# Optimization experiments

Hardware: AMD Instinct MI355X
Metric: run time of the kernel (lower is better)

The kernel has to match this reference:

```python
import jax, jax.numpy as jnp
import numpy as np
from jax import lax

S, B, XD, AD, ZD, K, H = 128, 32, 1024, 8, 4, 3, 50
CN = 32 * 3 * 3
DN = ('NCHW', 'OIHW', 'NCHW')


def setup_inputs():
    key = jax.random.key(0)
    ks = jax.random.split(key, 20)
    g = lambda k, sh, s=0.1: jax.random.normal(k, sh, dtype=jnp.float32) * s
    z = lambda n: jnp.zeros((n,), jnp.float32)
    return {
        'x': jax.random.uniform(ks[0], (S, B, XD), dtype=jnp.float32),
        'eps': jax.random.normal(ks[1], (S, B, AD), dtype=jnp.float32),
        'Wc0': g(ks[2], (32, 1, 3, 3)), 'bc0': z(32),
        'Wc1': g(ks[3], (32, 32, 3, 3)), 'bc1': z(32),
        'Wc2': g(ks[4], (32, 32, 3, 3)), 'bc2': z(32),
        'Wm': g(ks[5], (AD, CN)), 'bm': z(AD),
        'Wlv': g(ks[6], (AD, CN)), 'blv': z(AD),
        'Wd': g(ks[7], (CN, AD)), 'bd': z(CN),
        'Wt0': g(ks[8], (32, 32, 3, 3)), 'bt0': z(32),
        'Wt1': g(ks[9], (32, 32, 3, 3)), 'bt1': z(32),
        'Wt2': g(ks[10], (32, 32, 3, 3)), 'bt2': z(32),
        'Wg': g(ks[11], (32, 1, 1, 1)), 'bg': z(1),
        'A': jnp.tile(jnp.eye(ZD, dtype=jnp.float32)[None], (K, 1, 1)),
        'Bm': g(ks[12], (K, ZD, AD), 0.05),
        'Cm': g(ks[13], (K, AD, ZD), 0.05),
        'a_init': jnp.zeros((1, AD), jnp.float32),
        'W_ih': g(ks[14], (4 * H, AD)), 'W_hh': g(ks[15], (4 * H, H)),
        'b_ih': z(4 * H), 'b_hh': z(4 * H),
        'Wa': g(ks[16], (K, H)), 'ba': z(K),
    }


def _conv(h, W, b):
    y = lax.conv_general_dilated(h, W, (2, 2), 'VALID', dimension_numbers=DN)
    return y + b[None, :, None, None]


def _convT(h, W, b, op):
    # PyTorch ConvTranspose2d(k=3, stride=2, padding=0, output_padding=op)
    Wf = jnp.transpose(jnp.flip(W, (2, 3)), (1, 0, 2, 3))
    pad = (2, 2 + op)
    y = lax.conv_general_dilated(h, Wf, (1, 1), [pad, pad], lhs_dilation=(2, 2), dimension_numbers=DN)
    return y + b[None, :, None, None]


def _forward(x, eps, Wc0, bc0, Wc1, bc1, Wc2, bc2, Wm, bm, Wlv, blv, Wd, bd,
             Wt0, bt0, Wt1, bt1, Wt2, bt2, Wg, bg, A, Bm, Cm, a_init,
             W_ih, W_hh, b_ih, b_hh, Wa, ba):
    relu, sig = jax.nn.relu, jax.nn.sigmoid
    # ---- encode: x -> a ----
    xf = x.reshape(S * B, 1, 32, 32)
    h = relu(_conv(xf, Wc0, bc0))          # (SB,32,15,15)
    h = relu(_conv(h, Wc1, bc1))           # (SB,32,7,7)
    h = relu(_conv(h, Wc2, bc2))           # (SB,32,3,3)
    feat = h.reshape(S, B, CN)
    a_mean = feat @ Wm.T + bm
    a_logvar = sig(feat @ Wlv.T + blv)
    a = a_mean + eps * jnp.exp(0.5 * a_logvar)
    # ---- decode: a -> log_y ----
    d = (a.reshape(S * B, AD) @ Wd.T + bd).reshape(S * B, 32, 3, 3)
    d = relu(_convT(d, Wt0, bt0, 0))       # (SB,32,7,7)
    d = relu(_convT(d, Wt1, bt1, 0))       # (SB,32,15,15)
    d = relu(_convT(d, Wt2, bt2, 1))       # (SB,32,32,32)
    log_y = sig(jnp.einsum('nchw,c->nhw', d, Wg[:, 0, 0, 0]) + bg[0]).reshape(S, B, XD)
    # ---- alpha from a_{t-1} via LSTM ----
    a_tm1 = jnp.concatenate([jnp.broadcast_to(a_init[:, None, :], (1, B, AD)), a[:-1]], 0)
    def lstm_step(carry, xt):
        h_, c_ = carry
        gates = xt @ W_ih.T + b_ih + h_ @ W_hh.T + b_hh
        i, f, gg, o = jnp.split(gates, 4, axis=-1)
        c_ = sig(f) * c_ + sig(i) * jnp.tanh(gg)
        h_ = sig(o) * jnp.tanh(c_)
        return (h_, c_), h_
    _, hs = lax.scan(lstm_step, (jnp.zeros((B, H), jnp.float32), jnp.zeros((B, H), jnp.float32)), a_tm1)
    alpha = jax.nn.softmax(hs @ Wa.T + ba, axis=-1)     # (S,B,K)
    A_mix = jnp.einsum('sbk,kij->sbij', alpha, A)
    B_mix = jnp.einsum('sbk,kij->sbij', alpha, Bm)
    C_mix = jnp.einsum('sbk,kij->sbij', alpha, Cm)
    u = a_tm1
    # ---- Kalman filter ----
    Qm = 0.08 * jnp.eye(ZD, dtype=jnp.float32)
    Rm = 0.03 * jnp.eye(AD, dtype=jnp.float32)
    Iz = jnp.eye(ZD, dtype=jnp.float32)
    mu0 = jnp.zeros((B, ZD), jnp.float32)
    Sigma0 = 20.0 * jnp.tile(Iz[None], (B, 1, 1))
    def filt(carry, xs):
        mu, Sig = carry
        A_t, B_t, C_t, a_t, u_t, first = xs
        mu_p = jnp.einsum('bij,bj->bi', A_t, mu) + jnp.einsum('bij,bj->bi', B_t, u_t)
        Sig_p = A_t @ Sig @ jnp.swapaxes(A_t, 1, 2) + Qm
        mu_p = jnp.where(first, mu0, mu_p)
        Sig_p = jnp.where(first, Sigma0, Sig_p)
        res = a_t - jnp.einsum('bij,bj->bi', C_t, mu_p)
        S_ = C_t @ Sig_p @ jnp.swapaxes(C_t, 1, 2) + Rm
        Kt = Sig_p @ jnp.swapaxes(C_t, 1, 2) @ jnp.linalg.inv(S_)
        mu_f = mu_p + jnp.einsum('bij,bj->bi', Kt, res)
        IKC = Iz - Kt @ C_t
        Sig_f = IKC @ Sig_p @ jnp.swapaxes(IKC, 1, 2) + Kt @ Rm @ jnp.swapaxes(Kt, 1, 2)
        return (mu_f, Sig_f), (mu_p, mu_f, Sig_p, Sig_f)
    first = jnp.arange(S) == 0
    _, (mu_pred, mu_filt, Sig_pred, Sig_filt) = lax.scan(filt, (mu0, Sigma0), (A_mix, B_mix, C_mix, a, u, first))
    # ---- RTS smoother ----
    def smooth(carry, xs):
        mu_s, Sig_s = carry
        Sf, A_n, Sp_n, muf, muf_n = xs
        J = Sf @ jnp.swapaxes(A_n, 1, 2) @ jnp.linalg.inv(Sp_n)
        mu_new = muf + jnp.einsum('bij,bj->bi', J, mu_s - muf_n)
        Sig_new = Sf + J @ (Sig_s - Sp_n) @ jnp.swapaxes(J, 1, 2)
        return (mu_new, Sig_new), (mu_new, Sig_new)
    _, (mu_sm, Sig_sm) = lax.scan(smooth, (mu_filt[-1], Sig_filt[-1]),
                                  (Sig_filt[:-1], A_mix[1:], Sig_pred[1:], mu_filt[:-1], mu_filt[1:]),
                                  reverse=True)
    mu_smooth = jnp.concatenate([mu_sm, mu_filt[-1:]], 0)
    Sigma_smooth = jnp.concatenate([Sig_sm, Sig_filt[-1:]], 0)
    return log_y, a, a_mean, a_logvar, mu_smooth, Sigma_smooth


def reference(x, eps, Wc0, bc0, Wc1, bc1, Wc2, bc2, Wm, bm, Wlv, blv, Wd, bd,
              Wt0, bt0, Wt1, bt1, Wt2, bt2, Wg, bg, A, Bm, Cm, a_init,
              W_ih, W_hh, b_ih, b_hh, Wa, ba):
    return _forward(x, eps, Wc0, bc0, Wc1, bc1, Wc2, bc2, Wm, bm, Wlv, blv, Wd, bd,
                    Wt0, bt0, Wt1, bt1, Wt2, bt2, Wg, bg, A, Bm, Cm, a_init,
                    W_ih, W_hh, b_ih, b_hh, Wa, ba)
```

## Files before the change

kernel.cpp:

```cpp
#include <hip/hip_runtime.h>
#include <math.h>

#define DI __device__ __forceinline__

DI float sigm(float x){ return 1.0f/(1.0f+__expf(-x)); }
DI float tanhx(float x){ float ax=fabsf(x); float e=__expf(2.0f*ax); float t=1.0f-2.0f/(e+1.0f); return copysignf(t,x); }
DI unsigned short f2bf(float x){ unsigned u=__float_as_uint(x); return (unsigned short)((u+0x7fffu+((u>>16)&1u))>>16); }

typedef __attribute__((ext_vector_type(8))) short bf16x8;
typedef __attribute__((ext_vector_type(4))) float f32x4;
#define MFMA16(a,b,c) __builtin_amdgcn_mfma_f32_16x16x32_bf16(a,b,c,0,0,0)

static constexpr int RS  = 296;
static constexpr int RSZ = 9472;
static constexpr int AS  = 40;

static constexpr size_t OFF_A   = 4194304;
static constexpr size_t OFF_AM  = OFF_A   + 32768;
static constexpr size_t OFF_ALV = OFF_AM  + 32768;
static constexpr size_t OFF_MU  = OFF_ALV + 32768;
static constexpr size_t OFF_SG  = OFF_MU  + 16384;

DI float inv4_lane(float Mv, int r, int c){
  int a0=(c==0)?1:0, a1=(c<=1)?2:1, a2=(c<=2)?3:2;
  int b0=(r==0)?1:0, b1=(r<=1)?2:1, b2=(r<=2)?3:2;
  float m00=__shfl(Mv,(a0<<3)|b0,64), m01=__shfl(Mv,(a0<<3)|b1,64), m02=__shfl(Mv,(a0<<3)|b2,64);
  float m10=__shfl(Mv,(a1<<3)|b0,64), m11=__shfl(Mv,(a1<<3)|b1,64), m12=__shfl(Mv,(a1<<3)|b2,64);
  float m20=__shfl(Mv,(a2<<3)|b0,64), m21=__shfl(Mv,(a2<<3)|b1,64), m22=__shfl(Mv,(a2<<3)|b2,64);
  float det3 = m00*(m11*m22-m12*m21) - m01*(m10*m22-m12*m20) + m02*(m10*m21-m11*m20);
  float adj = (((r+c)&1)? -det3 : det3);
  float det=0.f;
  #pragma unroll
  for(int i=0;i<4;i++)
    det += __shfl(Mv,(i<<3),64)*__shfl(adj,i,64);
  return adj*(1.0f/det);
}

DI void inv4_serial(const float* m, float* o){
  float i0 = m[5]*m[10]*m[15]-m[5]*m[11]*m[14]-m[9]*m[6]*m[15]+m[9]*m[7]*m[14]+m[13]*m[6]*m[11]-m[13]*m[7]*m[10];
  float i4 = -m[4]*m[10]*m[15]+m[4]*m[11]*m[14]+m[8]*m[6]*m[15]-m[8]*m[7]*m[14]-m[12]*m[6]*m[11]+m[12]*m[7]*m[10];
  float i8 = m[4]*m[9]*m[15]-m[4]*m[11]*m[13]-m[8]*m[5]*m[15]+m[8]*m[7]*m[13]+m[12]*m[5]*m[11]-m[12]*m[7]*m[9];
  float i12= -m[4]*m[9]*m[14]+m[4]*m[10]*m[13]+m[8]*m[5]*m[14]-m[8]*m[6]*m[13]-m[12]*m[5]*m[10]+m[12]*m[6]*m[9];
  float i1 = -m[1]*m[10]*m[15]+m[1]*m[11]*m[14]+m[9]*m[2]*m[15]-m[9]*m[3]*m[14]-m[13]*m[2]*m[11]+m[13]*m[3]*m[10];
  float i5 = m[0]*m[10]*m[15]-m[0]*m[11]*m[14]-m[8]*m[2]*m[15]+m[8]*m[3]*m[14]+m[12]*m[2]*m[11]-m[12]*m[3]*m[10];
  float i9 = -m[0]*m[9]*m[15]+m[0]*m[11]*m[13]+m[8]*m[1]*m[15]-m[8]*m[3]*m[13]-m[12]*m[1]*m[11]+m[12]*m[3]*m[9];
  float i13= m[0]*m[9]*m[14]-m[0]*m[10]*m[13]-m[8]*m[1]*m[14]+m[8]*m[2]*m[13]+m[12]*m[1]*m[10]-m[12]*m[2]*m[9];
  float i2 = m[1]*m[6]*m[15]-m[1]*m[7]*m[14]-m[5]*m[2]*m[15]+m[5]*m[3]*m[14]+m[13]*m[2]*m[7]-m[13]*m[3]*m[6];
  float i6 = -m[0]*m[6]*m[15]+m[0]*m[7]*m[14]+m[4]*m[2]*m[15]-m[4]*m[3]*m[14]-m[12]*m[2]*m[7]+m[12]*m[3]*m[6];
  float i10= m[0]*m[5]*m[15]-m[0]*m[7]*m[13]-m[4]*m[1]*m[15]+m[4]*m[3]*m[13]+m[12]*m[1]*m[7]-m[12]*m[3]*m[5];
  float i14= -m[0]*m[5]*m[14]+m[0]*m[6]*m[13]+m[4]*m[1]*m[14]-m[4]*m[2]*m[13]-m[12]*m[1]*m[6]+m[12]*m[2]*m[5];
  float i3 = -m[1]*m[6]*m[11]+m[1]*m[7]*m[10]+m[5]*m[2]*m[11]-m[5]*m[3]*m[10]-m[9]*m[2]*m[7]+m[9]*m[3]*m[6];
  float i7 = m[0]*m[6]*m[11]-m[0]*m[7]*m[10]-m[4]*m[2]*m[11]+m[4]*m[3]*m[10]+m[8]*m[2]*m[7]-m[8]*m[3]*m[6];
  float i11= -m[0]*m[5]*m[11]+m[0]*m[7]*m[9]+m[4]*m[1]*m[11]-m[4]*m[3]*m[9]-m[8]*m[1]*m[7]+m[8]*m[3]*m[5];
  float i15= m[0]*m[5]*m[10]-m[0]*m[6]*m[9]-m[4]*m[1]*m[10]+m[4]*m[2]*m[9]+m[8]*m[1]*m[6]-m[8]*m[2]*m[5];
  float rd=1.0f/(m[0]*i0+m[1]*i4+m[2]*i8+m[3]*i12);
  o[0]=i0*rd; o[1]=i1*rd; o[2]=i2*rd; o[3]=i3*rd;
  o[4]=i4*rd; o[5]=i5*rd; o[6]=i6*rd; o[7]=i7*rd;
  o[8]=i8*rd; o[9]=i9*rd; o[10]=i10*rd; o[11]=i11*rd;
  o[12]=i12*rd; o[13]=i13*rd; o[14]=i14*rd; o[15]=i15*rd;
}

__global__ __launch_bounds__(256) void k_prep(
    const float* __restrict__ Wc1, const float* __restrict__ Wc2,
    const float* __restrict__ Wt0, const float* __restrict__ Wt1, const float* __restrict__ Wt2,
    unsigned short* __restrict__ ws16)
{
  int idx = blockIdx.x*256 + threadIdx.x;
  int mat = idx/RSZ, rem = idx%RSZ;
  int co = rem/RS, t = rem%RS;
  float v = 0.f;
  if (t < 288){
    int tap = t>>5, ci = t&31;
    if      (mat==0) v = Wc1[co*288+ci*9+tap];
    else if (mat==1) v = Wc2[co*288+ci*9+tap];
    else if (mat==2) v = Wt0[ci*288+co*9+tap];
    else if (mat==3) v = Wt1[ci*288+co*9+tap];
    else             v = Wt2[ci*288+co*9+tap];
  }
  ws16[idx] = f2bf(v);
}

struct EncSh {
  alignas(16) float img[1024];
  alignas(16) unsigned short h0T[9040];
  alignas(16) unsigned short h1T[2000];
  alignas(16) unsigned short BT1e[9472];
  alignas(16) unsigned short BT2e[9472];
  alignas(16) float feat[288];
};

__global__ __launch_bounds__(256) void k_enc(
    const float* __restrict__ x, const float* __restrict__ eps,
    const float* __restrict__ Wc0, const float* __restrict__ bc0,
    const float* __restrict__ bc1, const float* __restrict__ bc2,
    const float* __restrict__ Wm, const float* __restrict__ bm,
    const float* __restrict__ Wlv, const float* __restrict__ blv,
    const unsigned short* __restrict__ ws16,
    float* __restrict__ out)
{
  __shared__ EncSh E;
  const int n = blockIdx.x, tid = threadIdx.x;
  const int lane = tid & 63, wave = tid >> 6, g = lane >> 4, c15 = lane & 15;

  for (int i=tid;i<1024;i+=256) E.img[i]=x[(size_t)n*1024+i];
  {
    uint4* dst=(uint4*)E.BT1e;
    const uint4* src=(const uint4*)ws16;
    for (int i=tid;i<2368;i+=256) dst[i]=src[i];
  }
  if (tid<32){ E.h0T[225*AS+tid]=0; E.h1T[49*AS+tid]=0; }
  __syncthreads();

  for (int i=tid;i<7200;i+=256){
    int co=i&31, p=i>>5, oy=p/15, ox=p%15;
    float acc=bc0[co];
    const float* wp=Wc0+co*9;
    int base=2*oy*32+2*ox;
    #pragma unroll
    for(int ky=0;ky<3;ky++)
      #pragma unroll
      for(int kx=0;kx<3;kx++)
        acc += E.img[base+ky*32+kx]*wp[ky*3+kx];
    E.h0T[p*AS+co]=f2bf(fmaxf(acc,0.0f));
  }
  __syncthreads();

  {
    const int mt=wave;
    const int oy=mt*2+(c15>>3), ox=c15&7;
    f32x4 acc0={0.f,0.f,0.f,0.f}, acc1={0.f,0.f,0.f,0.f};
    #pragma unroll 1
    for (int ky=0;ky<3;ky++){
      #pragma unroll
      for (int kx=0;kx<3;kx++){
        int iy=2*oy+ky, ix=2*ox+kx;
        int pix=(iy<15&&ix<15)?(iy*15+ix):225;
        bf16x8 af=*(const bf16x8*)&E.h0T[pix*AS+g*8];
        int tap=ky*3+kx;
        bf16x8 b0=*(const bf16x8*)&E.BT1e[c15*RS+tap*32+g*8];
        bf16x8 b1=*(const bf16x8*)&E.BT1e[(c15+16)*RS+tap*32+g*8];
        acc0=MFMA16(af,b0,acc0);
        acc1=MFMA16(af,b1,acc1);
      }
    }
    float bA=bc1[c15], bB=bc1[c15+16];
    #pragma unroll
    for (int r=0;r<4;r++){
      int p16=g*4+r, oy2=mt*2+(p16>>3), ox2=p16&7;
      if (oy2<7 && ox2<7){
        E.h1T[(oy2*7+ox2)*AS+c15]   =f2bf(fmaxf(acc0[r]+bA,0.f));
        E.h1T[(oy2*7+ox2)*AS+c15+16]=f2bf(fmaxf(acc1[r]+bB,0.f));
      }
    }
  }
  __syncthreads();

  if (wave<2){
    const int nt=wave;
    const int valid=(c15<9);
    const int oy=c15/3, ox=c15-oy*3;
    f32x4 acc={0.f,0.f,0.f,0.f};
    #pragma unroll 1
    for (int ky=0;ky<3;ky++){
      #pragma unroll
      for (int kx=0;kx<3;kx++){
        int pix=valid?((2*oy+ky)*7+(2*ox+kx)):49;
        bf16x8 af=*(const bf16x8*)&E.h1T[pix*AS+g*8];
        int tap=ky*3+kx;
        bf16x8 bfr=*(const bf16x8*)&E.BT2e[(nt*16+c15)*RS+tap*32+g*8];
        acc=MFMA16(af,bfr,acc);
      }
    }
    float bb=bc2[nt*16+c15];
    #pragma unroll
    for (int r=0;r<4;r++){
      int p16=g*4+r;
      if (p16<9) E.feat[(nt*16+c15)*9+p16]=fmaxf(acc[r]+bb,0.f);
    }
  }
  __syncthreads();

  if (tid<64){
    const int j=tid>>3, kk=tid&7;
    float s1=0.f,s2=0.f;
    const float* wm=Wm+j*288;
    const float* wl=Wlv+j*288;
    #pragma unroll 6
    for(int m=kk*36;m<kk*36+36;m++){ float f=E.feat[m]; s1+=f*wm[m]; s2+=f*wl[m]; }
    #pragma unroll
    for(int d=4;d>0;d>>=1){ s1+=__shfl_down(s1,d,64); s2+=__shfl_down(s2,d,64); }
    if(kk==0){
      size_t o=(size_t)n*8+j;
      float am=s1+bm[j];
      float lv=sigm(s2+blv[j]);
      float av=am+eps[o]*__expf(0.5f*lv);
      out[OFF_AM+o]=am;
      out[OFF_ALV+o]=lv;
      out[OFF_A+o]=av;
    }
  }
}

struct DecSh {
  alignas(16) float aa[8];
  alignas(16) unsigned short d0T[400];
  alignas(16) unsigned short t0T[2000];
  alignas(16) unsigned short t1T[9040];
  alignas(16) unsigned short BT0[9472];
  alignas(16) unsigned short BT1[9472];
  alignas(16) unsigned short BT2[9472];
};
struct SeqSh {
  float a_loc[1024];
  float a0[8];
  float h[52];
  float gates[200];
  float wa[152];
  float w2[8][60];
  float logit[4];
  float alpha[384];
  float muf[512];
  float Sigf[2048];
  float Sigp[2048];
  float Jb[2048];
  float Amat[48];
};
union MainSh { DecSh d; SeqSh q; };

DI void kf_step(SeqSh& Q, int ks, int r, int c, bool aid,
                float At3[3], float Bt3[3], float Ct3[3],
                float& mu0, float& mu1, float& mu2, float& mu3, float& Sg)
{
  float al0=Q.alpha[ks*3+0], al1=Q.alpha[ks*3+1], al2=Q.alpha[ks*3+2];
  float At=al0*At3[0]+al1*At3[1]+al2*At3[2];
  float Bt=al0*Bt3[0]+al1*Bt3[1]+al2*Bt3[2];
  float Ct=al0*Ct3[0]+al1*Ct3[1]+al2*Ct3[2];
  float Mc=0.f;
  #pragma unroll
  for(int m=0;m<8;m++) Mc+=__shfl(Ct,(m<<3)|r,64)*__shfl(Ct,(m<<3)|c,64);
  float mp0,mp1,mp2,mp3;
  {
    float uc=(ks==0)?Q.a0[c]:Q.a_loc[(ks-1)*8+c];
    float vB=Bt*uc;
    vB+=__shfl_xor(vB,1,64); vB+=__shfl_xor(vB,2,64); vB+=__shfl_xor(vB,4,64);
    if (aid){
      mp0=mu0+__shfl(vB,0,64); mp1=mu1+__shfl(vB,8,64);
      mp2=mu2+__shfl(vB,16,64); mp3=mu3+__shfl(vB,24,64);
    } else {
      float mcc=(c==0)?mu0:((c==1)?mu1:((c==2)?mu2:((c==3)?mu3:0.f)));
      float vA=At*mcc;
      vA+=__shfl_xor(vA,1,64); vA+=__shfl_xor(vA,2,64);
      float comb=vA+vB;
      mp0=__shfl(comb,0,64); mp1=__shfl(comb,8,64);
      mp2=__shfl(comb,16,64); mp3=__shfl(comb,24,64);
    }
  }
  float Sp;
  if (aid){
    Sp=Sg+((r==c)?0.08f:0.f);
  } else {
    float T=0.f;
    #pragma unroll
    for(int k=0;k<4;k++) T+=__shfl(At,(r<<3)|k,64)*__shfl(Sg,(k<<3)|c,64);
    float sp=0.f;
    #pragma unroll
    for(int k=0;k<4;k++) sp+=__shfl(T,(r<<3)|k,64)*__shfl(At,(c<<3)|k,64);
    Sp=sp+((r==c)?0.08f:0.f);
  }
  if (ks==0){ mp0=0;mp1=0;mp2=0;mp3=0; Sp=(r==c)?20.f:0.f; }
  if (r<4&&c<4) Q.Sigp[ks*16+r*4+c]=Sp;
  float rr;
  {
    float mpc=(c==0)?mp0:((c==1)?mp1:((c==2)?mp2:((c==3)?mp3:0.f)));
    float v=Ct*mpc;
    v+=__shfl_xor(v,1,64); v+=__shfl_xor(v,2,64);
    rr=Q.a_loc[ks*8+r]-v;
  }
  float Spi=inv4_lane(Sp,r,c);
  float Mm=Spi+Mc*(1.0f/0.03f);
  float Sf=inv4_lane(Mm,r,c);
  if (r<4&&c<4) Q.Sigf[ks*16+r*4+c]=Sf;
  float Kq=0.f;
  #pragma unroll
  for(int k=0;k<4;k++) Kq+=__shfl(Sf,(r<<3)|k,64)*__shfl(Ct,(c<<3)|k,64);
  Kq*=(1.0f/0.03f);
  float resc=__shfl(rr,c<<3,64);
  float vv=Kq*resc;
  vv+=__shfl_xor(vv,1,64); vv+=__shfl_xor(vv,2,64); vv+=__shfl_xor(vv,4,64);
  float mufr=((r==0)?mp0:((r==1)?mp1:((r==2)?mp2:mp3)))+vv;
  float nm0=__shfl(mufr,0,64), nm1=__shfl(mufr,8,64), nm2=__shfl(mufr,16,64), nm3=__shfl(mufr,24,64);
  if (r<4&&c==0) Q.muf[ks*4+r]=mufr;
  mu0=nm0; mu1=nm1; mu2=nm2; mu3=nm3; Sg=Sf;
}

__global__ __launch_bounds__(512) void k_main(
    const float* __restrict__ Wd, const float* __restrict__ bd,
    const float* __restrict__ bt0, const float* __restrict__ bt1, const float* __restrict__ bt2,
    const float* __restrict__ Wg, const float* __restrict__ bgp,
    const float* __restrict__ Ag, const float* __restrict__ Bg, const float* __restrict__ Cg,
    const float* __restrict__ a_init,
    const float* __restrict__ W_ih, const float* __restrict__ W_hh,
    const float* __restrict__ b_ih, const float* __restrict__ b_hh,
    const float* __restrict__ Wa, const float* __restrict__ ba,
    const unsigned short* __restrict__ ws16,
    float* __restrict__ out)
{
  __shared__ MainSh sh;
  const int tid=threadIdx.x;
  const float* aglob = out + OFF_A;

  if (blockIdx.x < 32){
    if (tid>=256) return;
    SeqSh& Q = sh.q;
    const int b=blockIdx.x;
    for (int i=tid;i<1024;i+=256){ int s=i>>3, j=i&7; Q.a_loc[i]=aglob[((size_t)s*32+b)*8+j]; }
    if (tid<8)   Q.a0[tid]=a_init[tid];
    if (tid<150) Q.wa[tid]=Wa[tid];
    if (tid<52)  Q.h[tid]=0.f;
    if (tid>=208 && tid<256) Q.Amat[tid-208]=Ag[tid-208];
    for (int i=tid;i<464;i+=256){
      int rr2=i/58, k=i%58;
      Q.w2[rr2][k]=(k<8)? W_ih[(192+rr2)*8+k] : W_hh[(192+rr2)*50+(k-8)];
    }
    if (tid<8) Q.w2[tid][58]=b_ih[192+tid]+b_hh[192+tid];

    const int gr = tid-64;
    float wr[50], wi[8], bsum=0.f, creg=0.f;
    if (tid>=64){
      #pragma unroll
      for(int k=0;k<50;k++) wr[k]=W_hh[gr*50+k];
      #pragma unroll
      for(int j=0;j<8;j++) wi[j]=W_ih[gr*8+j];
      bsum=b_ih[gr]+b_hh[gr];
    }
    const int r=tid>>3, c=tid&7;
    float At3[3]={0,0,0}, Bt3[3]={0,0,0}, Ct3[3]={0,0,0};
    float mu0=0,mu1=0,mu2=0,mu3=0, Sg=0.f;
    bool aid=false;
    if (tid<64){
      if (r<4&&c<4){ At3[0]=Ag[r*4+c]; At3[1]=Ag[16+r*4+c]; At3[2]=Ag[32+r*4+c]; }
      if (r<4){ Bt3[0]=Bg[r*8+c]; Bt3[1]=Bg[32+r*8+c]; Bt3[2]=Bg[64+r*8+c]; }
      if (c<4){ Ct3[0]=Cg[r*4+c]; Ct3[1]=Cg[32+r*4+c]; Ct3[2]=Cg[64+r*4+c]; }
      int ok=1;
      if (r<4&&c<4){
        float d=(r==c)?1.f:0.f;
        ok=(At3[0]==d)&&(At3[1]==d)&&(At3[2]==d);
      }
      aid=(bool)__all(ok);
    }
    __syncthreads();

    for (int s=0;s<128;s++){
      if (tid>=64){
        float aA=bsum, aB=0.f;
        const float* ap=(s==0)?Q.a0:(Q.a_loc+(s-1)*8);
        #pragma unroll
        for(int j=0;j<8;j++) aA+=ap[j]*wi[j];
        #pragma unroll
        for(int k=0;k<50;k+=2){ aA+=Q.h[k]*wr[k]; aB+=Q.h[k+1]*wr[k+1]; }
        Q.gates[gr]=aA+aB;
        if (gr<8){
          const float* wp=Q.w2[gr];
          float s2=wp[58];
          #pragma unroll
          for(int j=0;j<8;j++) s2+=ap[j]*wp[j];
          #pragma unroll 10
          for(int k=0;k<50;k++) s2+=Q.h[k]*wp[8+k];
          Q.gates[192+gr]=s2;
        } else if (gr>=16 && gr<19 && s>0){
          int j=gr-16;
          float lv=ba[j];
          const float* wap=&Q.wa[j*50];
          #pragma unroll 5
          for(int k=0;k<50;k++) lv+=Q.h[k]*wap[k];
          Q.logit[j]=lv;
        }
      } else if (s>=2){
        kf_step(Q,s-2,r,c,aid,At3,Bt3,Ct3,mu0,mu1,mu2,mu3,Sg);
      }
      __syncthreads();
      if (tid>=64 && tid<114){
        int j=gr;
        float ig=sigm(Q.gates[j]);
        float fg=sigm(Q.gates[50+j]);
        float gg=tanhx(Q.gates[100+j]);
        float og=sigm(Q.gates[150+j]);
        creg=fg*creg+ig*gg;
        Q.h[j]=og*tanhx(creg);
      } else if (tid>=114 && tid<117 && s>0){
        int j=tid-114;
        float l0=Q.logit[0], l1=Q.logit[1], l2=Q.logit[2];
        float mx=fmaxf(l0,fmaxf(l1,l2));
        float e0=__expf(l0-mx), e1=__expf(l1-mx), e2=__expf(l2-mx);
        float lj=(j==0)?l0:((j==1)?l1:l2);
        Q.alpha[(s-1)*3+j]=__expf(lj-mx)/(e0+e1+e2);
      }
      __syncthreads();
    }
    if (tid<64){
      kf_step(Q,126,r,c,aid,At3,Bt3,Ct3,mu0,mu1,mu2,mu3,Sg);
    } else if (tid<67){
      int j=tid-64;
      float lv=ba[j];
      const float* wap=&Q.wa[j*50];
      #pragma unroll 5
      for(int k=0;k<50;k++) lv+=Q.h[k]*wap[k];
      Q.logit[j]=lv;
    }
    __syncthreads();
    if (tid>=64 && tid<67){
      int j=tid-64;
      float l0=Q.logit[0], l1=Q.logit[1], l2=Q.logit[2];
      float mx=fmaxf(l0,fmaxf(l1,l2));
      float e0=__expf(l0-mx), e1=__expf(l1-mx), e2=__expf(l2-mx);
      float lj=(j==0)?l0:((j==1)?l1:l2);
      Q.alpha[127*3+j]=__expf(lj-mx)/(e0+e1+e2);
    }
    __syncthreads();
    if (tid<64) kf_step(Q,127,r,c,aid,At3,Bt3,Ct3,mu0,mu1,mu2,mu3,Sg);
    __syncthreads();
    if (tid<127){
      const int n2=tid;
      float al0=Q.alpha[(n2+1)*3+0], al1=Q.alpha[(n2+1)*3+1], al2=Q.alpha[(n2+1)*3+2];
      float An[16], Sp[16], Spi[16], Sf[16], T[16];
      #pragma unroll
      for(int k=0;k<16;k++){
        An[k]=al0*Q.Amat[k]+al1*Q.Amat[16+k]+al2*Q.Amat[32+k];
        Sp[k]=Q.Sigp[(n2+1)*16+k];
        Sf[k]=Q.Sigf[n2*16+k];
      }
      inv4_serial(Sp,Spi);
      #pragma unroll
      for(int r2=0;r2<4;r2++)
        #pragma unroll
        for(int c2=0;c2<4;c2++){
          float s2=0.f;
          #pragma unroll
          for(int k=0;k<4;k++) s2+=Sf[r2*4+k]*An[c2*4+k];
          T[r2*4+c2]=s2;
        }
      #pragma unroll
      for(int r2=0;r2<4;r2++)
        #pragma unroll
        for(int c2=0;c2<4;c2++){
          float s2=0.f;
          #pragma unroll
          for(int k=0;k<4;k++) s2+=T[r2*4+k]*Spi[k*4+c2];
          Q.Jb[n2*16+r2*4+c2]=s2;
        }
    }
    __syncthreads();
    if (tid<64){
      if (r<4&&c==0) out[OFF_MU+((size_t)127*32+b)*4+r]=Q.muf[127*4+r];
      if (r<4&&c<4)  out[OFF_SG+((size_t)127*32+b)*16+r*4+c]=Q.Sigf[127*16+r*4+c];
      float ms0=Q.muf[508], ms1=Q.muf[509], ms2=Q.muf[510], ms3=Q.muf[511];
      float Ss=(r<4&&c<4)?Q.Sigf[127*16+r*4+c]:0.f;
      for (int n2=126;n2>=0;n2--){
        float Jv =(r<4&&c<4)?Q.Jb[n2*16+r*4+c]:0.f;
        float Sfv=(r<4&&c<4)?Q.Sigf[n2*16+r*4+c]:0.f;
        float Spn=(r<4&&c<4)?Q.Sigp[(n2+1)*16+r*4+c]:0.f;
        float Dv=Ss-Spn;
        float T2=0.f;
        #pragma unroll
        for(int k=0;k<4;k++) T2+=__shfl(Jv,(r<<3)|k,64)*__shfl(Dv,(k<<3)|c,64);
        float Sn=Sfv;
        #pragma unroll
        for(int k=0;k<4;k++) Sn+=__shfl(T2,(r<<3)|k,64)*__shfl(Jv,(c<<3)|k,64);
        float dmc;
        {
          float msc=(c==0)?ms0:((c==1)?ms1:((c==2)?ms2:((c==3)?ms3:0.f)));
          float mfn=Q.muf[(n2+1)*4+((c<4)?c:0)];
          dmc=(c<4)?(msc-mfn):0.f;
        }
        float v=Jv*dmc;
        v+=__shfl_xor(v,1,64); v+=__shfl_xor(v,2,64);
        float munr=Q.muf[n2*4+((r<4)?r:0)]+v;
        if (r<4&&c==0) out[OFF_MU+((size_t)n2*32+b)*4+r]=munr;
        if (r<4&&c<4)  out[OFF_SG+((size_t)n2*32+b)*16+r*4+c]=Sn;
        ms0=__shfl(munr,0,64); ms1=__shfl(munr,8,64); ms2=__shfl(munr,16,64); ms3=__shfl(munr,24,64);
        Ss=Sn;
      }
    }
    return;
  }

  DecSh& D = sh.d;
  const int n = blockIdx.x - 32;
  const int lane = tid & 63, wave = tid >> 6, g = lane >> 4, c15 = lane & 15;

  if (tid<8) D.aa[tid]=aglob[(size_t)n*8+tid];
  {
    uint4* dst=(uint4*)D.BT0;
    const uint4* src=(const uint4*)(ws16 + 2*RSZ);
    for (int i=tid;i<3552;i+=512) dst[i]=src[i];
  }
  if (tid<32){ D.d0T[9*AS+tid]=0; D.t0T[49*AS+tid]=0; D.t1T[225*AS+tid]=0; }
  __syncthreads();
  if (tid<288){
    float acc=bd[tid];
    #pragma unroll
    for(int j=0;j<8;j++) acc+=D.aa[j]*Wd[tid*8+j];
    D.d0T[(tid%9)*AS+(tid/9)]=f2bf(acc);
  }
  __syncthreads();
  {
    const int mt=wave>>1, nt=wave&1;
    const int pa=mt*16+c15;
    const int oh=pa/7, ow=pa%7;
    const bool pv=(pa<49);
    f32x4 acc={0.f,0.f,0.f,0.f};
    #pragma unroll 1
    for (int kh=0;kh<3;kh++){
      int th=oh-kh;
      bool vh=pv && th>=0 && !(th&1) && th<=4;
      int ihb=(th>>1)*3;
      #pragma unroll
      for (int kw=0;kw<3;kw++){
        int tw=ow-kw;
        bool v=vh && tw>=0 && !(tw&1) && tw<=4;
        int pix=v?(ihb+(tw>>1)):9;
        bf16x8 af=*(const bf16x8*)&D.d0T[pix*AS+g*8];
        int tap=kh*3+kw;
        bf16x8 bb=*(const bf16x8*)&D.BT0[(nt*16+c15)*RS+tap*32+g*8];
        acc=MFMA16(af,bb,acc);
      }
    }
    float bz=bt0[nt*16+c15];
    #pragma unroll
    for (int r=0;r<4;r++){
      int pc=mt*16+g*4+r;
      if (pc<49) D.t0T[pc*AS+nt*16+c15]=f2bf(fmaxf(acc[r]+bz,0.f));
    }
  }
  __syncthreads();
  {
    float bA=bt1[c15], bB=bt1[c15+16];
    #pragma unroll 1
    for (int u2=0;u2<2;u2++){
      int unit=wave+u2*8;
      int cls=unit>>2, mt=unit&3;
      int ph=cls>>1, pw=cls&1;
      int ii=mt*2+(c15>>3), jj=c15&7;
      f32x4 acc0={0.f,0.f,0.f,0.f}, acc1={0.f,0.f,0.f,0.f};
      #pragma unroll 1
      for (int kh=ph;kh<3;kh+=2){
        int ih=ii-(kh>>1);
        #pragma unroll
        for (int kw=pw;kw<3;kw+=2){
          int iw=jj-(kw>>1);
          int pix=(ih>=0&&ih<7&&iw>=0&&iw<7)?(ih*7+iw):49;
          bf16x8 af=*(const bf16x8*)&D.t0T[pix*AS+g*8];
          int tap=kh*3+kw;
          bf16x8 b0=*(const bf16x8*)&D.BT1[c15*RS+tap*32+g*8];
          bf16x8 b1=*(const bf16x8*)&D.BT1[(c15+16)*RS+tap*32+g*8];
          acc0=MFMA16(af,b0,acc0);
          acc1=MFMA16(af,b1,acc1);
        }
      }
      #pragma unroll
      for (int r=0;r<4;r++){
        int p16=g*4+r;
        int iio=mt*2+(p16>>3), jjo=p16&7;
        int oh=2*iio+ph, ow=2*jjo+pw;
        if (oh<15 && ow<15){
          D.t1T[(oh*15+ow)*AS+c15]   =f2bf(fmaxf(acc0[r]+bA,0.f));
          D.t1T[(oh*15+ow)*AS+c15+16]=f2bf(fmaxf(acc1[r]+bB,0.f));
        }
      }
    }
  }
  __syncthreads();
  {
    float bt2a=bt2[c15], bt2b=bt2[c15+16], wga=Wg[c15], wgb=Wg[c15+16], bgv=bgp[0];
    #pragma unroll 1
    for (int u2=0;u2<2;u2++){
      int ii=wave+u2*8;
      #pragma unroll 1
      for (int cls=0;cls<4;cls++){
        int ph=cls>>1, pw=cls&1;
        f32x4 acc0={0.f,0.f,0.f,0.f}, acc1={0.f,0.f,0.f,0.f};
        #pragma unroll 1
        for (int kh=ph;kh<3;kh+=2){
          int ih=ii-(kh>>1);
          if (ih<0||ih>14) continue;
          #pragma unroll
          for (int kw=pw;kw<3;kw+=2){
            int iw=c15-(kw>>1);
            int pix=(iw>=0&&iw<15)?(ih*15+iw):225;
            bf16x8 af=*(const bf16x8*)&D.t1T[pix*AS+g*8];
            int tap=kh*3+kw;
            bf16x8 b0=*(const bf16x8*)&D.BT2[c15*RS+tap*32+g*8];
            bf16x8 b1=*(const bf16x8*)&D.BT2[(c15+16)*RS+tap*32+g*8];
            acc0=MFMA16(af,b0,acc0);
            acc1=MFMA16(af,b1,acc1);
          }
        }
        int oh=2*ii+ph;
        float s0=fmaxf(acc0[0]+bt2a,0.f)*wga+fmaxf(acc1[0]+bt2b,0.f)*wgb;
        float s1=fmaxf(acc0[1]+bt2a,0.f)*wga+fmaxf(acc1[1]+bt2b,0.f)*wgb;
        float s2=fmaxf(acc0[2]+bt2a,0.f)*wga+fmaxf(acc1[2]+bt2b,0.f)*wgb;
        float s3=fmaxf(acc0[3]+bt2a,0.f)*wga+fmaxf(acc1[3]+bt2b,0.f)*wgb;
        #pragma unroll
        for (int d=1;d<16;d<<=1){
          s0+=__shfl_xor(s0,d,64); s1+=__shfl_xor(s1,d,64);
          s2+=__shfl_xor(s2,d,64); s3+=__shfl_xor(s3,d,64);
        }
        if (c15==0){
          size_t ob=(size_t)n*1024+(size_t)oh*32+pw;
          out[ob+2*(g*4+0)]=sigm(s0+bgv);
          out[ob+2*(g*4+1)]=sigm(s1+bgv);
          out[ob+2*(g*4+2)]=sigm(s2+bgv);
          out[ob+2*(g*4+3)]=sigm(s3+bgv);
        }
      }
    }
  }
}

extern "C" void kernel_launch(void* const* d_in, const int* in_sizes, int n_in,
                              void* d_out, int out_size, void* d_ws, size_t ws_size,
                              hipStream_t stream)
{
  const float* x    =(const float*)d_in[0];
  const float* eps  =(const float*)d_in[1];
  const float* Wc0  =(const float*)d_in[2];
  const float* bc0  =(const float*)d_in[3];
  const float* Wc1  =(const float*)d_in[4];
  const float* bc1  =(const float*)d_in[5];
  const float* Wc2  =(const float*)d_in[6];
  const float* bc2  =(const float*)d_in[7];
  const float* Wm   =(const float*)d_in[8];
  const float* bm   =(const float*)d_in[9];
  const float* Wlv  =(const float*)d_in[10];
  const float* blv  =(const float*)d_in[11];
  const float* Wd   =(const float*)d_in[12];
  const float* bd   =(const float*)d_in[13];
  const float* Wt0  =(const float*)d_in[14];
  const float* bt0  =(const float*)d_in[15];
  const float* Wt1  =(const float*)d_in[16];
  const float* bt1  =(const float*)d_in[17];
  const float* Wt2  =(const float*)d_in[18];
  const float* bt2  =(const float*)d_in[19];
  const float* Wg   =(const float*)d_in[20];
  const float* bg   =(const float*)d_in[21];
  const float* A    =(const float*)d_in[22];
  const float* Bm   =(const float*)d_in[23];
  const float* Cm   =(const float*)d_in[24];
  const float* a0   =(const float*)d_in[25];
  const float* W_ih =(const float*)d_in[26];
  const float* W_hh =(const float*)d_in[27];
  const float* b_ih =(const float*)d_in[28];
  const float* b_hh =(const float*)d_in[29];
  const float* Wa   =(const float*)d_in[30];
  const float* ba   =(const float*)d_in[31];
  float* out=(float*)d_out;
  unsigned short* ws16=(unsigned short*)d_ws;

  k_prep<<<185,256,0,stream>>>(Wc1,Wc2,Wt0,Wt1,Wt2,ws16);
  k_enc<<<4096,256,0,stream>>>(x,eps,Wc0,bc0,bc1,bc2,Wm,bm,Wlv,blv,ws16,out);
  k_main<<<4128,512,0,stream>>>(Wd,bd,bt0,bt1,bt2,Wg,bg,A,Bm,Cm,a0,
                                W_ih,W_hh,b_ih,b_hh,Wa,ba,ws16,out);
}
```

Measured before the change: 368.8 us.

## Split fused sequence/decoder kernel into separate launches with register-resident LSTM weights

Splits the merged k_main kernel into k_seq (32 blocks of 320 threads) for the LSTM/Kalman recurrence and k_dec (4096 blocks) for the decoder, launched in order on the same stream. The sequence kernel gets its own smaller shared-memory footprint, keeps all 200 gate rows and the 3 attention rows in registers, reads h with float4 using four accumulators, and prefetches the next smoother step's operands. Separating the kernels removes the union shared-memory sizing and lets the decoder run at its own occupancy. The cost is that the decoder blocks can no longer overlap with the serial sequence blocks, because the second launch waits for the first to finish.

```diff
diff --git a/kernel.cpp b/kernel.cpp
--- a/kernel.cpp
+++ b/kernel.cpp
@@ -201,22 +201,11 @@
   }
 }
 
-struct DecSh {
-  alignas(16) float aa[8];
-  alignas(16) unsigned short d0T[400];
-  alignas(16) unsigned short t0T[2000];
-  alignas(16) unsigned short t1T[9040];
-  alignas(16) unsigned short BT0[9472];
-  alignas(16) unsigned short BT1[9472];
-  alignas(16) unsigned short BT2[9472];
-};
 struct SeqSh {
-  float a_loc[1024];
-  float a0[8];
-  float h[52];
+  alignas(16) float a_loc[1024];
+  alignas(16) float a0[8];
+  alignas(16) float h[56];
   float gates[200];
-  float wa[152];
-  float w2[8][60];
   float logit[4];
   float alpha[384];
   float muf[512];
@@ -225,7 +214,6 @@
   float Jb[2048];
   float Amat[48];
 };
-union MainSh { DecSh d; SeqSh q; };
 
 DI void kf_step(SeqSh& Q, int ks, int r, int c, bool aid,
                 float At3[3], float Bt3[3], float Ct3[3],
@@ -293,199 +281,222 @@
   mu0=nm0; mu1=nm1; mu2=nm2; mu3=nm3; Sg=Sf;
 }
 
-__global__ __launch_bounds__(512) void k_main(
-    const float* __restrict__ Wd, const float* __restrict__ bd,
-    const float* __restrict__ bt0, const float* __restrict__ bt1, const float* __restrict__ bt2,
-    const float* __restrict__ Wg, const float* __restrict__ bgp,
+__global__ __launch_bounds__(320) void k_seq(
     const float* __restrict__ Ag, const float* __restrict__ Bg, const float* __restrict__ Cg,
     const float* __restrict__ a_init,
     const float* __restrict__ W_ih, const float* __restrict__ W_hh,
     const float* __restrict__ b_ih, const float* __restrict__ b_hh,
     const float* __restrict__ Wa, const float* __restrict__ ba,
-    const unsigned short* __restrict__ ws16,
     float* __restrict__ out)
 {
-  __shared__ MainSh sh;
+  __shared__ SeqSh Q;
   const int tid=threadIdx.x;
+  const int b=blockIdx.x;
   const float* aglob = out + OFF_A;
 
-  if (blockIdx.x < 32){
-    if (tid>=256) return;
-    SeqSh& Q = sh.q;
-    const int b=blockIdx.x;
-    for (int i=tid;i<1024;i+=256){ int s=i>>3, j=i&7; Q.a_loc[i]=aglob[((size_t)s*32+b)*8+j]; }
-    if (tid<8)   Q.a0[tid]=a_init[tid];
-    if (tid<150) Q.wa[tid]=Wa[tid];
-    if (tid<52)  Q.h[tid]=0.f;
-    if (tid>=208 && tid<256) Q.Amat[tid-208]=Ag[tid-208];
-    for (int i=tid;i<464;i+=256){
-      int rr2=i/58, k=i%58;
-      Q.w2[rr2][k]=(k<8)? W_ih[(192+rr2)*8+k] : W_hh[(192+rr2)*50+(k-8)];
-    }
-    if (tid<8) Q.w2[tid][58]=b_ih[192+tid]+b_hh[192+tid];
-
-    const int gr = tid-64;
-    float wr[50], wi[8], bsum=0.f, creg=0.f;
-    if (tid>=64){
-      #pragma unroll
-      for(int k=0;k<50;k++) wr[k]=W_hh[gr*50+k];
-      #pragma unroll
-      for(int j=0;j<8;j++) wi[j]=W_ih[gr*8+j];
-      bsum=b_ih[gr]+b_hh[gr];
-    }
-    const int r=tid>>3, c=tid&7;
-    float At3[3]={0,0,0}, Bt3[3]={0,0,0}, Ct3[3]={0,0,0};
-    float mu0=0,mu1=0,mu2=0,mu3=0, Sg=0.f;
-    bool aid=false;
-    if (tid<64){
-      if (r<4&&c<4){ At3[0]=Ag[r*4+c]; At3[1]=Ag[16+r*4+c]; At3[2]=Ag[32+r*4+c]; }
-      if (r<4){ Bt3[0]=Bg[r*8+c]; Bt3[1]=Bg[32+r*8+c]; Bt3[2]=Bg[64+r*8+c]; }
-      if (c<4){ Ct3[0]=Cg[r*4+c]; Ct3[1]=Cg[32+r*4+c]; Ct3[2]=Cg[64+r*4+c]; }
-      int ok=1;
-      if (r<4&&c<4){
-        float d=(r==c)?1.f:0.f;
-        ok=(At3[0]==d)&&(At3[1]==d)&&(At3[2]==d);
-      }
-      aid=(bool)__all(ok);
+  for (int i=tid;i<1024;i+=320){ int s=i>>3, j=i&7; Q.a_loc[i]=aglob[((size_t)s*32+b)*8+j]; }
+  if (tid<8)  Q.a0[tid]=a_init[tid];
+  if (tid<56) Q.h[tid]=0.f;
+  for (int i=tid;i<48;i+=320) Q.Amat[i]=Ag[i];
+
+  const int gr = tid-64;
+  float wr[52], wi[8], bsum=0.f, creg=0.f;
+  if (tid>=64 && tid<264){
+    #pragma unroll
+    for(int k=0;k<50;k++) wr[k]=W_hh[gr*50+k];
+    wr[50]=0.f; wr[51]=0.f;
+    #pragma unroll
+    for(int j=0;j<8;j++) wi[j]=W_ih[gr*8+j];
+    bsum=b_ih[gr]+b_hh[gr];
+  }
+  float wl[52]; float bl=0.f;
+  if (tid>=264 && tid<267){
+    #pragma unroll
+    for(int k=0;k<50;k++) wl[k]=Wa[(tid-264)*50+k];
+    wl[50]=0.f; wl[51]=0.f;
+    bl=ba[tid-264];
+  }
+  const int r=tid>>3, c=tid&7;
+  float At3[3]={0,0,0}, Bt3[3]={0,0,0}, Ct3[3]={0,0,0};
+  float mu0=0,mu1=0,mu2=0,mu3=0, Sg=0.f;
+  bool aid=false;
+  if (tid<64){
+    if (r<4&&c<4){ At3[0]=Ag[r*4+c]; At3[1]=Ag[16+r*4+c]; At3[2]=Ag[32+r*4+c]; }
+    if (r<4){ Bt3[0]=Bg[r*8+c]; Bt3[1]=Bg[32+r*8+c]; Bt3[2]=Bg[64+r*8+c]; }
+    if (c<4){ Ct3[0]=Cg[r*4+c]; Ct3[1]=Cg[32+r*4+c]; Ct3[2]=Cg[64+r*4+c]; }
+    int ok=1;
+    if (r<4&&c<4){
+      float d=(r==c)?1.f:0.f;
+      ok=(At3[0]==d)&&(At3[1]==d)&&(At3[2]==d);
+    }
+    aid=(bool)__all(ok);
+  }
+  __syncthreads();
+
+  for (int s=0;s<128;s++){
+    if (tid>=64 && tid<264){
+      const float* ap=(s==0)?Q.a0:(Q.a_loc+(s-1)*8);
+      float4 av0=*(const float4*)ap, av1=*(const float4*)(ap+4);
+      float aA=bsum+av0.x*wi[0]+av0.y*wi[1]+av0.z*wi[2]+av0.w*wi[3]
+                   +av1.x*wi[4]+av1.y*wi[5]+av1.z*wi[6]+av1.w*wi[7];
+      float aB=0.f,aC=0.f,aD=0.f;
+      #pragma unroll
+      for(int q=0;q<13;q++){
+        float4 hv=*(const float4*)&Q.h[4*q];
+        aA+=hv.x*wr[4*q]; aB+=hv.y*wr[4*q+1]; aC+=hv.z*wr[4*q+2]; aD+=hv.w*wr[4*q+3];
+      }
+      Q.gates[gr]=(aA+aB)+(aC+aD);
+    } else if (tid>=264 && tid<267){
+      if (s>0){
+        float aA=bl,aB=0.f,aC=0.f,aD=0.f;
+        #pragma unroll
+        for(int q=0;q<13;q++){
+          float4 hv=*(const float4*)&Q.h[4*q];
+          aA+=hv.x*wl[4*q]; aB+=hv.y*wl[4*q+1]; aC+=hv.z*wl[4*q+2]; aD+=hv.w*wl[4*q+3];
+        }
+        Q.logit[tid-264]=(aA+aB)+(aC+aD);
+      }
+    } else if (tid<64){
+      if (s>=2) kf_step(Q,s-2,r,c,aid,At3,Bt3,Ct3,mu0,mu1,mu2,mu3,Sg);
     }
     __syncthreads();
-
-    for (int s=0;s<128;s++){
-      if (tid>=64){
-        float aA=bsum, aB=0.f;
-        const float* ap=(s==0)?Q.a0:(Q.a_loc+(s-1)*8);
-        #pragma unroll
-        for(int j=0;j<8;j++) aA+=ap[j]*wi[j];
-        #pragma unroll
-        for(int k=0;k<50;k+=2){ aA+=Q.h[k]*wr[k]; aB+=Q.h[k+1]*wr[k+1]; }
-        Q.gates[gr]=aA+aB;
-        if (gr<8){
-          const float* wp=Q.w2[gr];
-          float s2=wp[58];
-          #pragma unroll
-          for(int j=0;j<8;j++) s2+=ap[j]*wp[j];
-          #pragma unroll 10
-          for(int k=0;k<50;k++) s2+=Q.h[k]*wp[8+k];
-          Q.gates[192+gr]=s2;
-        } else if (gr>=16 && gr<19 && s>0){
-          int j=gr-16;
-          float lv=ba[j];
-          const float* wap=&Q.wa[j*50];
-          #pragma unroll 5
-          for(int k=0;k<50;k++) lv+=Q.h[k]*wap[k];
-          Q.logit[j]=lv;
-        }
-      } else if (s>=2){
-        kf_step(Q,s-2,r,c,aid,At3,Bt3,Ct3,mu0,mu1,mu2,mu3,Sg);
-      }
-      __syncthreads();
-      if (tid>=64 && tid<114){
-        int j=gr;
-        float ig=sigm(Q.gates[j]);
-        float fg=sigm(Q.gates[50+j]);
-        float gg=tanhx(Q.gates[100+j]);
-        float og=sigm(Q.gates[150+j]);
-        creg=fg*creg+ig*gg;
-        Q.h[j]=og*tanhx(creg);
-      } else if (tid>=114 && tid<117 && s>0){
-        int j=tid-114;
-        float l0=Q.logit[0], l1=Q.logit[1], l2=Q.logit[2];
-        float mx=fmaxf(l0,fmaxf(l1,l2));
-        float e0=__expf(l0-mx), e1=__expf(l1-mx), e2=__expf(l2-mx);
-        float lj=(j==0)?l0:((j==1)?l1:l2);
-        Q.alpha[(s-1)*3+j]=__expf(lj-mx)/(e0+e1+e2);
-      }
-      __syncthreads();
-    }
-    if (tid<64){
-      kf_step(Q,126,r,c,aid,At3,Bt3,Ct3,mu0,mu1,mu2,mu3,Sg);
-    } else if (tid<67){
-      int j=tid-64;
-      float lv=ba[j];
-      const float* wap=&Q.wa[j*50];
-      #pragma unroll 5
-      for(int k=0;k<50;k++) lv+=Q.h[k]*wap[k];
-      Q.logit[j]=lv;
-    }
-    __syncthreads();
-    if (tid>=64 && tid<67){
-      int j=tid-64;
+    if (tid>=64 && tid<114){
+      int j=gr;
+      float ig=sigm(Q.gates[j]);
+      float fg=sigm(Q.gates[50+j]);
+      float gg=tanhx(Q.gates[100+j]);
+      float og=sigm(Q.gates[150+j]);
+      creg=fg*creg+ig*gg;
+      Q.h[j]=og*tanhx(creg);
+    } else if (tid>=114 && tid<117 && s>0){
+      int j=tid-114;
       float l0=Q.logit[0], l1=Q.logit[1], l2=Q.logit[2];
       float mx=fmaxf(l0,fmaxf(l1,l2));
       float e0=__expf(l0-mx), e1=__expf(l1-mx), e2=__expf(l2-mx);
       float lj=(j==0)?l0:((j==1)?l1:l2);
-      Q.alpha[127*3+j]=__expf(lj-mx)/(e0+e1+e2);
+      Q.alpha[(s-1)*3+j]=__expf(lj-mx)/(e0+e1+e2);
     }
     __syncthreads();
-    if (tid<64) kf_step(Q,127,r,c,aid,At3,Bt3,Ct3,mu0,mu1,mu2,mu3,Sg);
-    __syncthreads();
-    if (tid<127){
-      const int n2=tid;
-      float al0=Q.alpha[(n2+1)*3+0], al1=Q.alpha[(n2+1)*3+1], al2=Q.alpha[(n2+1)*3+2];
-      float An[16], Sp[16], Spi[16], Sf[16], T[16];
-      #pragma unroll
-      for(int k=0;k<16;k++){
-        An[k]=al0*Q.Amat[k]+al1*Q.Amat[16+k]+al2*Q.Amat[32+k];
-        Sp[k]=Q.Sigp[(n2+1)*16+k];
-        Sf[k]=Q.Sigf[n2*16+k];
-      }
-      inv4_serial(Sp,Spi);
-      #pragma unroll
-      for(int r2=0;r2<4;r2++)
+  }
+  if (tid<64){
+    kf_step(Q,126,r,c,aid,At3,Bt3,Ct3,mu0,mu1,mu2,mu3,Sg);
+  } else if (tid>=264 && tid<267){
+    float aA=bl,aB=0.f,aC=0.f,aD=0.f;
+    #pragma unroll
+    for(int q=0;q<13;q++){
+      float4 hv=*(const float4*)&Q.h[4*q];
+      aA+=hv.x*wl[4*q]; aB+=hv.y*wl[4*q+1]; aC+=hv.z*wl[4*q+2]; aD+=hv.w*wl[4*q+3];
+    }
+    Q.logit[tid-264]=(aA+aB)+(aC+aD);
+  }
+  __syncthreads();
+  if (tid>=64 && tid<67){
+    int j=tid-64;
+    float l0=Q.logit[0], l1=Q.logit[1], l2=Q.logit[2];
+    float mx=fmaxf(l0,fmaxf(l1,l2));
+    float e0=__expf(l0-mx), e1=__expf(l1-mx), e2=__expf(l2-mx);
+    float lj=(j==0)?l0:((j==1)?l1:l2);
+    Q.alpha[127*3+j]=__expf(lj-mx)/(e0+e1+e2);
+  }
+  __syncthreads();
+  if (tid<64) kf_step(Q,127,r,c,aid,At3,Bt3,Ct3,mu0,mu1,mu2,mu3,Sg);
+  __syncthreads();
+  if (tid<127){
+    const int n2=tid;
+    float al0=Q.alpha[(n2+1)*3+0], al1=Q.alpha[(n2+1)*3+1], al2=Q.alpha[(n2+1)*3+2];
+    float An[16], Sp[16], Spi[16], Sf[16], T[16];
+    #pragma unroll
+    for(int k=0;k<16;k++){
+      An[k]=al0*Q.Amat[k]+al1*Q.Amat[16+k]+al2*Q.Amat[32+k];
+      Sp[k]=Q.Sigp[(n2+1)*16+k];
+      Sf[k]=Q.Sigf[n2*16+k];
+    }
+    inv4_serial(Sp,Spi);
+    #pragma unroll
+    for(int r2=0;r2<4;r2++)
+      #pragma unroll
+      for(int c2=0;c2<4;c2++){
+        float s2=0.f;
         #pragma unroll
-        for(int c2=0;c2<4;c2++){
-          float s2=0.f;
-          #pragma unroll
-          for(int k=0;k<4;k++) s2+=Sf[r2*4+k]*An[c2*4+k];
-          T[r2*4+c2]=s2;
-        }
-      #pragma unroll
-      for(int r2=0;r2<4;r2++)
+        for(int k=0;k<4;k++) s2+=Sf[r2*4+k]*An[c2*4+k];
+        T[r2*4+c2]=s2;
+      }
+    #pragma unroll
+    for(int r2=0;r2<4;r2++)
+      #pragma unroll
+      for(int c2=0;c2<4;c2++){
+        float s2=0.f;
         #pragma unroll
-        for(int c2=0;c2<4;c2++){
-          float s2=0.f;
-          #pragma unroll
-          for(int k=0;k<4;k++) s2+=T[r2*4+k]*Spi[k*4+c2];
-          Q.Jb[n2*16+r2*4+c2]=s2;
-        }
-    }
-    __syncthreads();
-    if (tid<64){
-      if (r<4&&c==0) out[OFF_MU+((size_t)127*32+b)*4+r]=Q.muf[127*4+r];
-      if (r<4&&c<4)  out[OFF_SG+((size_t)127*32+b)*16+r*4+c]=Q.Sigf[127*16+r*4+c];
-      float ms0=Q.muf[508], ms1=Q.muf[509], ms2=Q.muf[510], ms3=Q.muf[511];
-      float Ss=(r<4&&c<4)?Q.Sigf[127*16+r*4+c]:0.f;
-      for (int n2=126;n2>=0;n2--){
-        float Jv =(r<4&&c<4)?Q.Jb[n2*16+r*4+c]:0.f;
-        float Sfv=(r<4&&c<4)?Q.Sigf[n2*16+r*4+c]:0.f;
-        float Spn=(r<4&&c<4)?Q.Sigp[(n2+1)*16+r*4+c]:0.f;
-        float Dv=Ss-Spn;
-        float T2=0.f;
-        #pragma unroll
-        for(int k=0;k<4;k++) T2+=__shfl(Jv,(r<<3)|k,64)*__shfl(Dv,(k<<3)|c,64);
-        float Sn=Sfv;
-        #pragma unroll
-        for(int k=0;k<4;k++) Sn+=__shfl(T2,(r<<3)|k,64)*__shfl(Jv,(c<<3)|k,64);
-        float dmc;
-        {
-          float msc=(c==0)?ms0:((c==1)?ms1:((c==2)?ms2:((c==3)?ms3:0.f)));
-          float mfn=Q.muf[(n2+1)*4+((c<4)?c:0)];
-          dmc=(c<4)?(msc-mfn):0.f;
-        }
-        float v=Jv*dmc;
-        v+=__shfl_xor(v,1,64); v+=__shfl_xor(v,2,64);
-        float munr=Q.muf[n2*4+((r<4)?r:0)]+v;
-        if (r<4&&c==0) out[OFF_MU+((size_t)n2*32+b)*4+r]=munr;
-        if (r<4&&c<4)  out[OFF_SG+((size_t)n2*32+b)*16+r*4+c]=Sn;
-        ms0=__shfl(munr,0,64); ms1=__shfl(munr,8,64); ms2=__shfl(munr,16,64); ms3=__shfl(munr,24,64);
-        Ss=Sn;
-      }
-    }
-    return;
-  }
-
-  DecSh& D = sh.d;
-  const int n = blockIdx.x - 32;
+        for(int k=0;k<4;k++) s2+=T[r2*4+k]*Spi[k*4+c2];
+        Q.Jb[n2*16+r2*4+c2]=s2;
+      }
+  }
+  __syncthreads();
+  if (tid<64){
+    if (r<4&&c==0) out[OFF_MU+((size_t)127*32+b)*4+r]=Q.muf[127*4+r];
+    if (r<4&&c<4)  out[OFF_SG+((size_t)127*32+b)*16+r*4+c]=Q.Sigf[127*16+r*4+c];
+    float ms0=Q.muf[508], ms1=Q.muf[509], ms2=Q.muf[510], ms3=Q.muf[511];
+    float Ss=(r<4&&c<4)?Q.Sigf[127*16+r*4+c]:0.f;
+    const bool act=(r<4&&c<4);
+    float Jv = act?Q.Jb[126*16+r*4+c]:0.f;
+    float Sfv= act?Q.Sigf[126*16+r*4+c]:0.f;
+    float Spn= act?Q.Sigp[127*16+r*4+c]:0.f;
+    float mfn= Q.muf[127*4+((c<4)?c:0)];
+    float mfr= Q.muf[126*4+((r<4)?r:0)];
+    for (int n2=126;n2>=0;n2--){
+      float Jv2=0.f,Sfv2=0.f,Spn2=0.f,mfn2=0.f,mfr2=0.f;
+      if (n2>0){
+        Jv2 = act?Q.Jb[(n2-1)*16+r*4+c]:0.f;
+        Sfv2= act?Q.Sigf[(n2-1)*16+r*4+c]:0.f;
+        Spn2= act?Q.Sigp[n2*16+r*4+c]:0.f;
+        mfn2= Q.muf[n2*4+((c<4)?c:0)];
+        mfr2= Q.muf[(n2-1)*4+((r<4)?r:0)];
+      }
+      float Dv=Ss-Spn;
+      float T2=0.f;
+      #pragma unroll
+      for(int k=0;k<4;k++) T2+=__shfl(Jv,(r<<3)|k,64)*__shfl(Dv,(k<<3)|c,64);
+      float Sn=Sfv;
+      #pragma unroll
+      for(int k=0;k<4;k++) Sn+=__shfl(T2,(r<<3)|k,64)*__shfl(Jv,(c<<3)|k,64);
+      float dmc;
+      {
+        float msc=(c==0)?ms0:((c==1)?ms1:((c==2)?ms2:((c==3)?ms3:0.f)));
+        dmc=(c<4)?(msc-mfn):0.f;
+      }
+      float v=Jv*dmc;
+      v+=__shfl_xor(v,1,64); v+=__shfl_xor(v,2,64);
+      float munr=mfr+v;
+      if (r<4&&c==0) out[OFF_MU+((size_t)n2*32+b)*4+r]=munr;
+      if (act)       out[OFF_SG+((size_t)n2*32+b)*16+r*4+c]=Sn;
+      ms0=__shfl(munr,0,64); ms1=__shfl(munr,8,64); ms2=__shfl(munr,16,64); ms3=__shfl(munr,24,64);
+      Ss=Sn;
+      Jv=Jv2; Sfv=Sfv2; Spn=Spn2; mfn=mfn2; mfr=mfr2;
+    }
+  }
+}
+
+struct DecSh {
+  alignas(16) float aa[8];
+  alignas(16) unsigned short d0T[400];
+  alignas(16) unsigned short t0T[2000];
+  alignas(16) unsigned short t1T[9040];
+  alignas(16) unsigned short BT0[9472];
+  alignas(16) unsigned short BT1[9472];
+  alignas(16) unsigned short BT2[9472];
+};
+
+__global__ __launch_bounds__(512) void k_dec(
+    const float* __restrict__ Wd, const float* __restrict__ bd,
+    const float* __restrict__ bt0, const float* __restrict__ bt1, const float* __restrict__ bt2,
+    const float* __restrict__ Wg, const float* __restrict__ bgp,
+    const unsigned short* __restrict__ ws16,
+    float* __restrict__ out)
+{
+  __shared__ DecSh D;
+  const int tid=threadIdx.x;
+  const int n = blockIdx.x;
+  const float* aglob = out + OFF_A;
   const int lane = tid & 63, wave = tid >> 6, g = lane >> 4, c15 = lane & 15;
 
   if (tid<8) D.aa[tid]=aglob[(size_t)n*8+tid];
@@ -658,6 +669,6 @@
 
   k_prep<<<185,256,0,stream>>>(Wc1,Wc2,Wt0,Wt1,Wt2,ws16);
   k_enc<<<4096,256,0,stream>>>(x,eps,Wc0,bc0,bc1,bc2,Wm,bm,Wlv,blv,ws16,out);
-  k_main<<<4128,512,0,stream>>>(Wd,bd,bt0,bt1,bt2,Wg,bg,A,Bm,Cm,a0,
-                                W_ih,W_hh,b_ih,b_hh,Wa,ba,ws16,out);
-}
+  k_seq<<<32,320,0,stream>>>(A,Bm,Cm,a0,W_ih,W_hh,b_ih,b_hh,Wa,ba,out);
+  k_dec<<<4096,512,0,stream>>>(Wd,bd,bt0,bt1,bt2,Wg,bg,ws16,out);
+}
```

Result: slower. 428.1 us (+16.1%).
